# Kernel tuning notes

Measured on AMD Instinct MI355X. Metric: run time of the kernel, lower is better.

Reference implementation:

```python
import jax, jax.numpy as jnp
import numpy as np

K, MU, SIGMA = 8, 0.0, 0.1
M, N, D_DIM, T = 512, 1024, 512, 4096


def setup_inputs() -> dict:
    key = jax.random.key(0)
    ks, ke, ka, kd, kl1, kl2 = jax.random.split(key, 6)
    S = jax.random.normal(ks, (N, T), dtype=jnp.float32)
    E = jax.random.normal(ke, (M, T), dtype=jnp.float32)  # raw noise; scaled by sigma/mu in reference
    A = jax.random.uniform(ka, (M, N), dtype=jnp.float32)  # torch.rand init
    Dm = jax.random.normal(kd, (N, D_DIM), dtype=jnp.float32) / jnp.sqrt(N)  # stands in for DCT-transformed randn
    c = jnp.ones((1,), dtype=jnp.float32)
    l1 = 0.1 * jnp.abs(jax.random.normal(kl1, (1,), dtype=jnp.float32)) + 0.05
    l2 = jax.random.normal(kl2, (1,), dtype=jnp.float32)
    # LISTA params per layer; all K layers get the same closed-form init in the original
    U1 = jnp.eye(D_DIM, dtype=jnp.float32) - (1.0 / c[0]) * (Dm.T @ A.T @ A @ Dm)  # [d,d]
    V1 = (1.0 / c[0]) * (Dm.T @ A.T)  # [d,m]
    U = jnp.broadcast_to(U1, (K, D_DIM, D_DIM)).copy()
    V = jnp.broadcast_to(V1, (K, D_DIM, M)).copy()
    H0 = jnp.zeros((D_DIM, T), dtype=jnp.float32)
    return {"S": S, "E": E, "A": A, "D": Dm, "U": U, "V": V, "l1": l1, "l2": l2, "c": c, "H0": H0}


def reference(S, E, A, D, U, V, l1, l2, c, H0):
    # X = A @ S + noise (E ~ randn, scaled as in torch forward)
    X = A @ S + (E * SIGMA + MU)  # [m,T]
    # Self-attention on H0 (the original loop always feeds self.H, the zero buffer,
    # into every layer -- H is never chained). Attention map = softmax((D@H0)^T (D@H0)).
    G = D @ H0                                   # [n,T]
    attn = jax.nn.softmax(G.T @ G, axis=-1)      # [T,T]
    Z = l2[0] * (H0 @ attn)                      # [d,T]
    # All K LISTA updates share the same (H0-derived) Z and X -> batch over layers.
    mat = jnp.einsum('kde,et->kdt', U, Z) + jnp.einsum('kdm,mt->kdt', V, X)  # [K,d,T]
    thres = l1[0] / c[0]
    H_all = jnp.sign(mat) * jnp.maximum(jnp.zeros((), mat.dtype), jnp.abs(mat) - thres)
    H_last = H_all[-1]                           # only the last layer's H survives the loop
    return D @ H_last                            # S_star [n,T]
```

## Files before the change

### kernel.cpp

```cpp
#include <hip/hip_runtime.h>

typedef unsigned short ushort_t;
typedef unsigned int u32;
typedef ushort_t u16x8 __attribute__((ext_vector_type(8)));
typedef ushort_t u16x4 __attribute__((ext_vector_type(4)));
typedef __bf16   bf16x8 __attribute__((ext_vector_type(8)));
typedef float    f32x4  __attribute__((ext_vector_type(4)));

#define T_DIM 4096

__device__ __forceinline__ ushort_t f2bf(float f){
  union { float f; unsigned u; } x; x.f = f;
  unsigned r = x.u + 0x7FFFu + ((x.u >> 16) & 1u);
  return (ushort_t)(r >> 16);
}

__device__ __forceinline__ void gload16(const void* g, void* l){
  __builtin_amdgcn_global_load_lds(
      (const __attribute__((address_space(1))) u32*)g,
      (__attribute__((address_space(3))) u32*)l, 16, 0, 0);
}

__global__ __launch_bounds__(256) void prep_kernel(
    const float* __restrict__ S, const float* __restrict__ A,
    const float* __restrict__ V7, const float* __restrict__ Dm,
    ushort_t* __restrict__ St, ushort_t* __restrict__ Abf,
    ushort_t* __restrict__ Vbf, ushort_t* __restrict__ Dbf)
{
  __shared__ float tile[64][65];
  const int bid = blockIdx.x, tid = threadIdx.x;
  if (bid < 1024){
    const int t0 = (bid & 63) * 64, n0 = (bid >> 6) * 64;
#pragma unroll
    for (int i = 0; i < 4; ++i){
      int g = tid + 256 * i; int row = g >> 4, cq = g & 15;
      const f32x4 v = *(const f32x4*)&S[(size_t)(n0 + row) * T_DIM + t0 + cq * 4];
#pragma unroll
      for (int j = 0; j < 4; ++j) tile[row][cq * 4 + j] = v[j];
    }
    __syncthreads();
#pragma unroll
    for (int i = 0; i < 2; ++i){
      int g = tid + 256 * i; int tl = g >> 3, nq = g & 7;
      u16x8 h;
#pragma unroll
      for (int j = 0; j < 8; ++j) h[j] = f2bf(tile[nq * 8 + j][tl]);
      *(u16x8*)&St[(size_t)(t0 + tl) * 1024 + n0 + ((nq ^ (tl & 7)) << 3)] = h;
    }
  } else {
    int pid = bid - 1024;
    const float* src; ushort_t* dst; int g, ks;
    if (pid < 256)      { src = A;  dst = Abf; g = pid * 256 + tid;        ks = 7; }
    else if (pid < 384) { src = V7; dst = Vbf; g = (pid - 256) * 256 + tid; ks = 6; }
    else                { src = Dm; dst = Dbf; g = (pid - 384) * 256 + tid; ks = 6; }
    const int r = g >> ks, cg = g & ((1 << ks) - 1);
    const int Kd = 8 << ks;
    const size_t base = (size_t)r * Kd + (size_t)cg * 8;
    const f32x4 v0 = *(const f32x4*)&src[base];
    const f32x4 v1 = *(const f32x4*)&src[base + 4];
    u16x8 h;
#pragma unroll
    for (int j = 0; j < 4; ++j){ h[j] = f2bf(v0[j]); h[j + 4] = f2bf(v1[j]); }
    *(u16x8*)&dst[(size_t)r * Kd + ((cg >> 3) << 6) + ((((cg & 7) ^ (r & 7))) << 3)] = h;
  }
}

template<int EPI, int NK>
__global__ __launch_bounds__(512, 2) void gemm_kernel(
    const ushort_t* __restrict__ Ag, const ushort_t* __restrict__ Bg,
    void* __restrict__ Cout, const float* __restrict__ Eptr,
    const float* __restrict__ l1p, const float* __restrict__ cp)
{
  constexpr int KD = NK * 64;
  constexpr bool SWAP = (EPI != 2);
  constexpr int P = SWAP ? 2 : 4;
  constexpr int Q = SWAP ? 4 : 2;
  __shared__ __align__(16) ushort_t As[4][128 * 64];
  __shared__ __align__(16) ushort_t Bs[4][64 * 64];
  const int tid = threadIdx.x;
  const int lane = tid & 63, wid = tid >> 6;
  const int g = wid >> 2;
  const int s = wid & 3;
  const int wm = s >> 1, wn = s & 1;
  const int lr = lane & 15, lq = lane >> 4;
  const int t0 = blockIdx.x * 128, n0 = blockIdx.y * 64;
  const int ltid = tid & 255;

  f32x4 acc[P][Q];
#pragma unroll
  for (int p = 0; p < P; ++p)
#pragma unroll
    for (int q = 0; q < Q; ++q) acc[p][q] = (f32x4){0.f, 0.f, 0.f, 0.f};

  auto stage = [&](int kt){
    const int slot = ((kt & 1) << 1) | ((kt >> 1) & 1);
#pragma unroll
    for (int i = 0; i < 4; ++i){
      int c = i * 256 + ltid;
      gload16(&Ag[(size_t)(t0 + (c >> 3)) * KD + kt * 64 + (c & 7) * 8],
              &As[slot][(i * 256 + (ltid & 192)) * 8]);
    }
#pragma unroll
    for (int i = 0; i < 2; ++i){
      int c = i * 256 + ltid;
      gload16(&Bg[(size_t)(n0 + (c >> 3)) * KD + kt * 64 + (c & 7) * 8],
              &Bs[slot][(i * 256 + (ltid & 192)) * 8]);
    }
  };

  auto compute = [&](int kt){
    const int slot = ((kt & 1) << 1) | ((kt >> 1) & 1);
#pragma unroll
    for (int ksv = 0; ksv < 2; ++ksv){
      const int kb = ksv * 4 + lq;
      bf16x8 a[4], bb[2];
#pragma unroll
      for (int mf = 0; mf < 4; ++mf){
        int r = wm * 64 + mf * 16 + lr;
        a[mf] = *(const bf16x8*)&As[slot][r * 64 + ((kb ^ (r & 7)) << 3)];
      }
#pragma unroll
      for (int nf = 0; nf < 2; ++nf){
        int r = wn * 32 + nf * 16 + lr;
        bb[nf] = *(const bf16x8*)&Bs[slot][r * 64 + ((kb ^ (r & 7)) << 3)];
      }
      __builtin_amdgcn_s_setprio(1);
      if constexpr (SWAP){
#pragma unroll
        for (int nf = 0; nf < 2; ++nf)
#pragma unroll
          for (int mf = 0; mf < 4; ++mf)
            acc[nf][mf] = __builtin_amdgcn_mfma_f32_16x16x32_bf16(
                bb[nf], a[mf], acc[nf][mf], 0, 0, 0);
      } else {
#pragma unroll
        for (int mf = 0; mf < 4; ++mf)
#pragma unroll
          for (int nf = 0; nf < 2; ++nf)
            acc[mf][nf] = __builtin_amdgcn_mfma_f32_16x16x32_bf16(
                a[mf], bb[nf], acc[mf][nf], 0, 0, 0);
      }
      __builtin_amdgcn_s_setprio(0);
    }
  };

  if (g == 0){ stage(0); stage(2); }
  else       { stage(1); }

  for (int kt = 0; kt < NK; ++kt){
    if ((kt & 1) == g){
      if (kt + 2 < NK) { asm volatile("s_waitcnt vmcnt(6)" ::: "memory"); }
      else             { asm volatile("s_waitcnt vmcnt(0)" ::: "memory"); }
    }
    __builtin_amdgcn_s_barrier();
    __builtin_amdgcn_sched_barrier(0);
    if ((kt & 1) == g){
      compute(kt);
    } else {
      if (kt + 3 < NK) stage(kt + 3);
    }
  }

  float* red = (float*)&As[0][0];
  if (g == 1){
#pragma unroll
    for (int p = 0; p < P; ++p)
#pragma unroll
      for (int q = 0; q < Q; ++q)
        *(f32x4*)&red[s * 2048 + (p * Q + q) * 256 + lane * 4] = acc[p][q];
  }
  asm volatile("s_waitcnt lgkmcnt(0)" ::: "memory");
  __builtin_amdgcn_s_barrier();
  if (g == 0){
#pragma unroll
    for (int p = 0; p < P; ++p)
#pragma unroll
      for (int q = 0; q < Q; ++q){
        const f32x4 o = *(const f32x4*)&red[s * 2048 + (p * Q + q) * 256 + lane * 4];
        acc[p][q] += o;
      }

    if constexpr (EPI == 2){
      float* O = (float*)Cout;
#pragma unroll
      for (int mf = 0; mf < 4; ++mf)
#pragma unroll
        for (int nf = 0; nf < 2; ++nf){
          const int t = t0 + wm * 64 + mf * 16 + lq * 4;
          const int n = n0 + wn * 32 + nf * 16 + lr;
          *(f32x4*)&O[(size_t)n * T_DIM + t] = acc[mf][nf];
        }
    } else {
      const float thres = (EPI == 1) ? (l1p[0] / cp[0]) : 0.f;
      ushort_t* OT = (ushort_t*)Cout;
#pragma unroll
      for (int nf = 0; nf < 2; ++nf){
#pragma unroll
        for (int mf = 0; mf < 4; ++mf){
          const int m = n0 + wn * 32 + nf * 16 + lq * 4;
          const int t = t0 + wm * 64 + mf * 16 + lr;
          f32x4 v = acc[nf][mf];
          u16x4 h;
          if constexpr (EPI == 0){
#pragma unroll
            for (int j = 0; j < 4; ++j){
              float e = Eptr[(size_t)(m + j) * T_DIM + t];
              h[j] = f2bf(v[j] + 0.1f * e);
            }
          } else {
#pragma unroll
            for (int j = 0; j < 4; ++j){
              float av = fabsf(v[j]) - thres;
              float r = av > 0.f ? (v[j] > 0.f ? av : -av) : 0.f;
              h[j] = f2bf(r);
            }
          }
          *(u16x4*)&OT[(size_t)t * 512 + (m & ~63) +
                       (((((m >> 3) & 7) ^ (t & 7))) << 3) + (m & 7)] = h;
        }
      }
    }
  }
}

extern "C" void kernel_launch(void* const* d_in, const int* in_sizes, int n_in,
                              void* d_out, int out_size, void* d_ws, size_t ws_size,
                              hipStream_t stream)
{
  const float* S  = (const float*)d_in[0];
  const float* E  = (const float*)d_in[1];
  const float* A  = (const float*)d_in[2];
  const float* Dm = (const float*)d_in[3];
  const float* V  = (const float*)d_in[5];
  const float* l1 = (const float*)d_in[6];
  const float* c  = (const float*)d_in[8];

  char* ws = (char*)d_ws;
  ushort_t* St  = (ushort_t*)(ws);
  ushort_t* XT  = (ushort_t*)(ws + (size_t)( 8u << 20));
  ushort_t* HT  = (ushort_t*)(ws + (size_t)(12u << 20));
  ushort_t* Abf = (ushort_t*)(ws + (size_t)(16u << 20));
  ushort_t* Vbf = (ushort_t*)(ws + (size_t)(17u << 20));
  ushort_t* Dbf = (ushort_t*)(ws + (size_t)(17u << 20) + (512u << 10));
  const float* V7 = V + (size_t)7 * 512 * 512;

  prep_kernel<<<1664, 256, 0, stream>>>(S, A, V7, Dm, St, Abf, Vbf, Dbf);
  gemm_kernel<0, 16><<<dim3(32, 8), 512, 0, stream>>>(St, Abf, (void*)XT, E, nullptr, nullptr);
  gemm_kernel<1, 8><<<dim3(32, 8), 512, 0, stream>>>(XT, Vbf, (void*)HT, nullptr, l1, c);
  gemm_kernel<2, 8><<<dim3(32, 16), 512, 0, stream>>>(HT, Dbf, d_out, nullptr, nullptr, nullptr);
}
```

Measured before the change: 39.38 us.

## Fuse S transpose and bf16 conversion into first GEMM's staging loop

The separate prep pass that transposed S into a bf16 buffer is removed. The first GEMM now loads fp32 S tiles into registers, converts them to bf16 and writes them transposed into LDS, so the 16 MB St round trip disappears. The E noise tile is also prefetched into LDS asynchronously for the epilogue instead of being read from global memory with strided access. In exchange, staging now takes register-path loads and conversion work inside the pipelined loop, and each block adds 32 KB of LDS, which may reduce occupancy.

New measurement: 47.78 us. +21.3%, slower.

```diff
diff --git a/kernel.cpp b/kernel.cpp
--- a/kernel.cpp
+++ b/kernel.cpp
@@ -22,54 +22,175 @@
 }
 
 __global__ __launch_bounds__(256) void prep_kernel(
-    const float* __restrict__ S, const float* __restrict__ A,
-    const float* __restrict__ V7, const float* __restrict__ Dm,
-    ushort_t* __restrict__ St, ushort_t* __restrict__ Abf,
+    const float* __restrict__ A, const float* __restrict__ V7,
+    const float* __restrict__ Dm, ushort_t* __restrict__ Abf,
     ushort_t* __restrict__ Vbf, ushort_t* __restrict__ Dbf)
 {
-  __shared__ float tile[64][65];
-  const int bid = blockIdx.x, tid = threadIdx.x;
-  if (bid < 1024){
-    const int t0 = (bid & 63) * 64, n0 = (bid >> 6) * 64;
-#pragma unroll
-    for (int i = 0; i < 4; ++i){
-      int g = tid + 256 * i; int row = g >> 4, cq = g & 15;
-      const f32x4 v = *(const f32x4*)&S[(size_t)(n0 + row) * T_DIM + t0 + cq * 4];
-#pragma unroll
-      for (int j = 0; j < 4; ++j) tile[row][cq * 4 + j] = v[j];
-    }
-    __syncthreads();
+  const int pid = blockIdx.x, tid = threadIdx.x;
+  const float* src; ushort_t* dst; int g, ks;
+  if (pid < 256)      { src = A;  dst = Abf; g = pid * 256 + tid;        ks = 7; }
+  else if (pid < 384) { src = V7; dst = Vbf; g = (pid - 256) * 256 + tid; ks = 6; }
+  else                { src = Dm; dst = Dbf; g = (pid - 384) * 256 + tid; ks = 6; }
+  const int r = g >> ks, cg = g & ((1 << ks) - 1);
+  const int Kd = 8 << ks;
+  const size_t base = (size_t)r * Kd + (size_t)cg * 8;
+  const f32x4 v0 = *(const f32x4*)&src[base];
+  const f32x4 v1 = *(const f32x4*)&src[base + 4];
+  u16x8 h;
+#pragma unroll
+  for (int j = 0; j < 4; ++j){ h[j] = f2bf(v0[j]); h[j + 4] = f2bf(v1[j]); }
+  *(u16x8*)&dst[(size_t)r * Kd + ((cg >> 3) << 6) + ((((cg & 7) ^ (r & 7))) << 3)] = h;
+}
+
+__global__ __launch_bounds__(512, 2) void gemm1_kernel(
+    const float* __restrict__ S, const ushort_t* __restrict__ Bg,
+    const float* __restrict__ E, ushort_t* __restrict__ XT)
+{
+  constexpr int NK = 16;
+  __shared__ __align__(16) ushort_t As[4][128 * 64];
+  __shared__ __align__(16) ushort_t Bs[4][64 * 64];
+  __shared__ __align__(16) float Elds[64 * 128];
+  const int tid = threadIdx.x;
+  const int lane = tid & 63, wid = tid >> 6;
+  const int g = wid >> 2;
+  const int s = wid & 3;
+  const int wm = s >> 1, wn = s & 1;
+  const int lr = lane & 15, lq = lane >> 4;
+  const int t0 = blockIdx.x * 128, n0 = blockIdx.y * 64;
+  const int ltid = tid & 255;
+
+  f32x4 acc[2][4];
+#pragma unroll
+  for (int p = 0; p < 2; ++p)
+#pragma unroll
+    for (int q = 0; q < 4; ++q) acc[p][q] = (f32x4){0.f, 0.f, 0.f, 0.f};
+
+  auto stage = [&](int kt){
+    const int slot = ((kt & 1) << 1) | ((kt >> 1) & 1);
+    f32x4 rS[2][4];
 #pragma unroll
     for (int i = 0; i < 2; ++i){
-      int g = tid + 256 * i; int tl = g >> 3, nq = g & 7;
-      u16x8 h;
-#pragma unroll
-      for (int j = 0; j < 8; ++j) h[j] = f2bf(tile[nq * 8 + j][tl]);
-      *(u16x8*)&St[(size_t)(t0 + tl) * 1024 + n0 + ((nq ^ (tl & 7)) << 3)] = h;
-    }
-  } else {
-    int pid = bid - 1024;
-    const float* src; ushort_t* dst; int g, ks;
-    if (pid < 256)      { src = A;  dst = Abf; g = pid * 256 + tid;        ks = 7; }
-    else if (pid < 384) { src = V7; dst = Vbf; g = (pid - 256) * 256 + tid; ks = 6; }
-    else                { src = Dm; dst = Dbf; g = (pid - 384) * 256 + tid; ks = 6; }
-    const int r = g >> ks, cg = g & ((1 << ks) - 1);
-    const int Kd = 8 << ks;
-    const size_t base = (size_t)r * Kd + (size_t)cg * 8;
-    const f32x4 v0 = *(const f32x4*)&src[base];
-    const f32x4 v1 = *(const f32x4*)&src[base + 4];
-    u16x8 h;
-#pragma unroll
-    for (int j = 0; j < 4; ++j){ h[j] = f2bf(v0[j]); h[j + 4] = f2bf(v1[j]); }
-    *(u16x8*)&dst[(size_t)r * Kd + ((cg >> 3) << 6) + ((((cg & 7) ^ (r & 7))) << 3)] = h;
+      const int task = i * 256 + ltid, rg = task >> 5, tq = task & 31;
+#pragma unroll
+      for (int ii = 0; ii < 4; ++ii)
+        rS[i][ii] = *(const f32x4*)&S[(size_t)(kt * 64 + rg * 4 + ii) * T_DIM
+                                      + t0 + tq * 4];
+    }
+    __builtin_amdgcn_sched_barrier(0);
+#pragma unroll
+    for (int i = 0; i < 2; ++i){
+      int c = i * 256 + ltid;
+      gload16(&Bg[(size_t)(n0 + (c >> 3)) * 1024 + kt * 64 + (c & 7) * 8],
+              &Bs[slot][(i * 256 + (ltid & 192)) * 8]);
+    }
+    __builtin_amdgcn_sched_barrier(0);
+    asm volatile("s_waitcnt vmcnt(2)" ::: "memory");
+#pragma unroll
+    for (int i = 0; i < 2; ++i){
+      const int task = i * 256 + ltid, rg = task >> 5, tq = task & 31;
+#pragma unroll
+      for (int j = 0; j < 4; ++j){
+        const int t = tq * 4 + j;
+        u16x4 w;
+#pragma unroll
+        for (int ii = 0; ii < 4; ++ii) w[ii] = f2bf(rS[i][ii][j]);
+        *(u16x4*)&As[slot][t * 64 + (((rg >> 1) ^ ((t >> 1) & 7)) << 3)
+                           + ((rg & 1) << 2)] = w;
+      }
+    }
+    asm volatile("s_waitcnt lgkmcnt(0)" ::: "memory");
+  };
+
+  auto compute = [&](int kt){
+    const int slot = ((kt & 1) << 1) | ((kt >> 1) & 1);
+#pragma unroll
+    for (int ksv = 0; ksv < 2; ++ksv){
+      const int kb = ksv * 4 + lq;
+      bf16x8 a[4], bb[2];
+#pragma unroll
+      for (int mf = 0; mf < 4; ++mf){
+        int r = wm * 64 + mf * 16 + lr;
+        a[mf] = *(const bf16x8*)&As[slot][r * 64 + ((kb ^ ((r >> 1) & 7)) << 3)];
+      }
+#pragma unroll
+      for (int nf = 0; nf < 2; ++nf){
+        int r = wn * 32 + nf * 16 + lr;
+        bb[nf] = *(const bf16x8*)&Bs[slot][r * 64 + ((kb ^ (r & 7)) << 3)];
+      }
+      __builtin_amdgcn_s_setprio(1);
+#pragma unroll
+      for (int nf = 0; nf < 2; ++nf)
+#pragma unroll
+        for (int mf = 0; mf < 4; ++mf)
+          acc[nf][mf] = __builtin_amdgcn_mfma_f32_16x16x32_bf16(
+              bb[nf], a[mf], acc[nf][mf], 0, 0, 0);
+      __builtin_amdgcn_s_setprio(0);
+    }
+  };
+
+#pragma unroll
+  for (int i = 0; i < 4; ++i){
+    int c = i * 512 + tid;
+    gload16(&E[(size_t)(n0 + (c >> 5)) * T_DIM + t0 + (c & 31) * 4],
+            (char*)Elds + (size_t)(i * 512 + (tid & 448)) * 16);
+  }
+  __builtin_amdgcn_sched_barrier(0);
+  if (g == 0){ stage(0); stage(2); }
+  else       { stage(1); }
+
+  for (int kt = 0; kt < NK; ++kt){
+    __builtin_amdgcn_s_barrier();
+    __builtin_amdgcn_sched_barrier(0);
+    if ((kt & 1) == g){
+      compute(kt);
+    } else {
+      if (kt + 3 < NK) stage(kt + 3);
+      else             asm volatile("s_waitcnt vmcnt(0)" ::: "memory");
+    }
+  }
+
+  float* red = (float*)&As[0][0];
+  if (g == 1){
+#pragma unroll
+    for (int p = 0; p < 2; ++p)
+#pragma unroll
+      for (int q = 0; q < 4; ++q)
+        *(f32x4*)&red[s * 2048 + (p * 4 + q) * 256 + lane * 4] = acc[p][q];
+  }
+  asm volatile("s_waitcnt lgkmcnt(0)" ::: "memory");
+  __builtin_amdgcn_s_barrier();
+  if (g == 0){
+#pragma unroll
+    for (int p = 0; p < 2; ++p)
+#pragma unroll
+      for (int q = 0; q < 4; ++q)
+        acc[p][q] += *(const f32x4*)&red[s * 2048 + (p * 4 + q) * 256 + lane * 4];
+
+#pragma unroll
+    for (int nf = 0; nf < 2; ++nf){
+#pragma unroll
+      for (int mf = 0; mf < 4; ++mf){
+        const int m = n0 + wn * 32 + nf * 16 + lq * 4;
+        const int t = t0 + wm * 64 + mf * 16 + lr;
+        const int em = wn * 32 + nf * 16 + lq * 4;
+        const int tl = wm * 64 + mf * 16 + lr;
+        f32x4 v = acc[nf][mf];
+        u16x4 h;
+#pragma unroll
+        for (int j = 0; j < 4; ++j)
+          h[j] = f2bf(v[j] + 0.1f * Elds[(em + j) * 128 + tl]);
+        *(u16x4*)&XT[(size_t)t * 512 + (m & ~63) +
+                     (((((m >> 3) & 7) ^ (t & 7))) << 3) + (m & 7)] = h;
+      }
+    }
   }
 }
 
 template<int EPI, int NK>
 __global__ __launch_bounds__(512, 2) void gemm_kernel(
     const ushort_t* __restrict__ Ag, const ushort_t* __restrict__ Bg,
-    void* __restrict__ Cout, const float* __restrict__ Eptr,
-    const float* __restrict__ l1p, const float* __restrict__ cp)
+    void* __restrict__ Cout, const float* __restrict__ l1p,
+    const float* __restrict__ cp)
 {
   constexpr int KD = NK * 64;
   constexpr bool SWAP = (EPI != 2);
@@ -175,10 +296,8 @@
 #pragma unroll
     for (int p = 0; p < P; ++p)
 #pragma unroll
-      for (int q = 0; q < Q; ++q){
-        const f32x4 o = *(const f32x4*)&red[s * 2048 + (p * Q + q) * 256 + lane * 4];
-        acc[p][q] += o;
-      }
+      for (int q = 0; q < Q; ++q)
+        acc[p][q] += *(const f32x4*)&red[s * 2048 + (p * Q + q) * 256 + lane * 4];
 
     if constexpr (EPI == 2){
       float* O = (float*)Cout;
@@ -191,7 +310,7 @@
           *(f32x4*)&O[(size_t)n * T_DIM + t] = acc[mf][nf];
         }
     } else {
-      const float thres = (EPI == 1) ? (l1p[0] / cp[0]) : 0.f;
+      const float thres = l1p[0] / cp[0];
       ushort_t* OT = (ushort_t*)Cout;
 #pragma unroll
       for (int nf = 0; nf < 2; ++nf){
@@ -201,19 +320,11 @@
           const int t = t0 + wm * 64 + mf * 16 + lr;
           f32x4 v = acc[nf][mf];
           u16x4 h;
-          if constexpr (EPI == 0){
-#pragma unroll
-            for (int j = 0; j < 4; ++j){
-              float e = Eptr[(size_t)(m + j) * T_DIM + t];
-              h[j] = f2bf(v[j] + 0.1f * e);
-            }
-          } else {
-#pragma unroll
-            for (int j = 0; j < 4; ++j){
-              float av = fabsf(v[j]) - thres;
-              float r = av > 0.f ? (v[j] > 0.f ? av : -av) : 0.f;
-              h[j] = f2bf(r);
-            }
+#pragma unroll
+          for (int j = 0; j < 4; ++j){
+            float av = fabsf(v[j]) - thres;
+            float r = av > 0.f ? (v[j] > 0.f ? av : -av) : 0.f;
+            h[j] = f2bf(r);
           }
           *(u16x4*)&OT[(size_t)t * 512 + (m & ~63) +
                        (((((m >> 3) & 7) ^ (t & 7))) << 3) + (m & 7)] = h;
@@ -236,16 +347,15 @@
   const float* c  = (const float*)d_in[8];
 
   char* ws = (char*)d_ws;
-  ushort_t* St  = (ushort_t*)(ws);
-  ushort_t* XT  = (ushort_t*)(ws + (size_t)( 8u << 20));
-  ushort_t* HT  = (ushort_t*)(ws + (size_t)(12u << 20));
-  ushort_t* Abf = (ushort_t*)(ws + (size_t)(16u << 20));
-  ushort_t* Vbf = (ushort_t*)(ws + (size_t)(17u << 20));
-  ushort_t* Dbf = (ushort_t*)(ws + (size_t)(17u << 20) + (512u << 10));
+  ushort_t* XT  = (ushort_t*)(ws);
+  ushort_t* HT  = (ushort_t*)(ws + (size_t)( 4u << 20));
+  ushort_t* Abf = (ushort_t*)(ws + (size_t)( 8u << 20));
+  ushort_t* Vbf = (ushort_t*)(ws + (size_t)( 9u << 20));
+  ushort_t* Dbf = (ushort_t*)(ws + (size_t)(10u << 20));
   const float* V7 = V + (size_t)7 * 512 * 512;
 
-  prep_kernel<<<1664, 256, 0, stream>>>(S, A, V7, Dm, St, Abf, Vbf, Dbf);
-  gemm_kernel<0, 16><<<dim3(32, 8), 512, 0, stream>>>(St, Abf, (void*)XT, E, nullptr, nullptr);
-  gemm_kernel<1, 8><<<dim3(32, 8), 512, 0, stream>>>(XT, Vbf, (void*)HT, nullptr, l1, c);
-  gemm_kernel<2, 8><<<dim3(32, 16), 512, 0, stream>>>(HT, Dbf, d_out, nullptr, nullptr, nullptr);
-}
+  prep_kernel<<<640, 256, 0, stream>>>(A, V7, Dm, Abf, Vbf, Dbf);
+  gemm1_kernel<<<dim3(32, 8), 512, 0, stream>>>(S, Abf, E, XT);
+  gemm_kernel<1, 8><<<dim3(32, 8), 512, 0, stream>>>(XT, Vbf, (void*)HT, l1, c);
+  gemm_kernel<2, 8><<<dim3(32, 16), 512, 0, stream>>>(HT, Dbf, d_out, nullptr, nullptr);
+}
```

## Stage GEMM epilogue through LDS for coalesced stores and prefetch noise tile

Applied to the files above, without the earlier changes.

The GEMM epilogue now writes the reduced accumulators into LDS with the target swizzle applied, then has all 512 threads emit wide, contiguous global stores. Before, each lane wrote scattered 4-element fragments. For the X-producing GEMM, the noise tile E is loaded asynchronously into a new LDS buffer at kernel start, so the epilogue no longer does strided scalar global loads of E. The cost is extra LDS traffic, two more barriers in the epilogue, and an additional 32KB LDS buffer that raises shared-memory usage.

Measured after the change: 39.66 us. Within noise of the previous version (+0.7%).

```diff
diff --git a/kernel.cpp b/kernel.cpp
--- a/kernel.cpp
+++ b/kernel.cpp
@@ -77,6 +77,7 @@
   constexpr int Q = SWAP ? 4 : 2;
   __shared__ __align__(16) ushort_t As[4][128 * 64];
   __shared__ __align__(16) ushort_t Bs[4][64 * 64];
+  __shared__ __align__(16) float Elds[64 * 128];
   const int tid = threadIdx.x;
   const int lane = tid & 63, wid = tid >> 6;
   const int g = wid >> 2;
@@ -144,6 +145,15 @@
     }
   };
 
+  if constexpr (EPI == 0){
+#pragma unroll
+    for (int i = 0; i < 4; ++i){
+      int c = i * 512 + tid;
+      gload16(&Eptr[(size_t)(n0 + (c >> 5)) * T_DIM + t0 + (c & 31) * 4],
+              (char*)Elds + (size_t)(i * 512 + (tid & 448)) * 16);
+    }
+    __builtin_amdgcn_sched_barrier(0);
+  }
   if (g == 0){ stage(0); stage(2); }
   else       { stage(1); }
 
@@ -161,64 +171,95 @@
     }
   }
 
-  float* red = (float*)&As[0][0];
-  if (g == 1){
-#pragma unroll
-    for (int p = 0; p < P; ++p)
-#pragma unroll
-      for (int q = 0; q < Q; ++q)
-        *(f32x4*)&red[s * 2048 + (p * Q + q) * 256 + lane * 4] = acc[p][q];
-  }
-  asm volatile("s_waitcnt lgkmcnt(0)" ::: "memory");
-  __builtin_amdgcn_s_barrier();
-  if (g == 0){
-#pragma unroll
-    for (int p = 0; p < P; ++p)
-#pragma unroll
-      for (int q = 0; q < Q; ++q){
-        const f32x4 o = *(const f32x4*)&red[s * 2048 + (p * Q + q) * 256 + lane * 4];
-        acc[p][q] += o;
-      }
-
-    if constexpr (EPI == 2){
-      float* O = (float*)Cout;
-#pragma unroll
-      for (int mf = 0; mf < 4; ++mf)
-#pragma unroll
-        for (int nf = 0; nf < 2; ++nf){
-          const int t = t0 + wm * 64 + mf * 16 + lq * 4;
-          const int n = n0 + wn * 32 + nf * 16 + lr;
-          *(f32x4*)&O[(size_t)n * T_DIM + t] = acc[mf][nf];
-        }
-    } else {
+  float* accs = (float*)&As[0][0];
+
+  if constexpr (SWAP){
+    if (g == 1){
+#pragma unroll
+      for (int nf = 0; nf < 2; ++nf)
+#pragma unroll
+        for (int mf = 0; mf < 4; ++mf){
+          const int tl = wm * 64 + mf * 16 + lr;
+          const int em0 = wn * 32 + nf * 16 + lq * 4;
+          const int mp = (((em0 >> 3) ^ (tl & 7)) << 3) + (em0 & 7);
+          *(f32x4*)&accs[tl * 68 + mp] = acc[nf][mf];
+        }
+    }
+    asm volatile("s_waitcnt lgkmcnt(0)" ::: "memory");
+    __builtin_amdgcn_s_barrier();
+    if (g == 0){
       const float thres = (EPI == 1) ? (l1p[0] / cp[0]) : 0.f;
-      ushort_t* OT = (ushort_t*)Cout;
-#pragma unroll
-      for (int nf = 0; nf < 2; ++nf){
+#pragma unroll
+      for (int nf = 0; nf < 2; ++nf)
 #pragma unroll
         for (int mf = 0; mf < 4; ++mf){
-          const int m = n0 + wn * 32 + nf * 16 + lq * 4;
-          const int t = t0 + wm * 64 + mf * 16 + lr;
-          f32x4 v = acc[nf][mf];
-          u16x4 h;
+          const int tl = wm * 64 + mf * 16 + lr;
+          const int em0 = wn * 32 + nf * 16 + lq * 4;
+          const int mp = (((em0 >> 3) ^ (tl & 7)) << 3) + (em0 & 7);
+          f32x4 v = *(const f32x4*)&accs[tl * 68 + mp];
+          v += acc[nf][mf];
           if constexpr (EPI == 0){
 #pragma unroll
-            for (int j = 0; j < 4; ++j){
-              float e = Eptr[(size_t)(m + j) * T_DIM + t];
-              h[j] = f2bf(v[j] + 0.1f * e);
-            }
+            for (int j = 0; j < 4; ++j)
+              v[j] += 0.1f * Elds[(em0 + j) * 128 + tl];
           } else {
 #pragma unroll
             for (int j = 0; j < 4; ++j){
               float av = fabsf(v[j]) - thres;
-              float r = av > 0.f ? (v[j] > 0.f ? av : -av) : 0.f;
-              h[j] = f2bf(r);
+              v[j] = av > 0.f ? (v[j] > 0.f ? av : -av) : 0.f;
             }
           }
-          *(u16x4*)&OT[(size_t)t * 512 + (m & ~63) +
-                       (((((m >> 3) & 7) ^ (t & 7))) << 3) + (m & 7)] = h;
-        }
-      }
+          *(f32x4*)&accs[tl * 68 + mp] = v;
+        }
+    }
+    asm volatile("s_waitcnt lgkmcnt(0)" ::: "memory");
+    __builtin_amdgcn_s_barrier();
+    ushort_t* OT = (ushort_t*)Cout;
+#pragma unroll
+    for (int i = 0; i < 2; ++i){
+      const int c = i * 512 + tid;
+      const int t = c >> 3, mb = (c & 7) * 8;
+      const f32x4 a0 = *(const f32x4*)&accs[t * 68 + mb];
+      const f32x4 a1 = *(const f32x4*)&accs[t * 68 + mb + 4];
+      u16x8 h;
+#pragma unroll
+      for (int j = 0; j < 4; ++j){ h[j] = f2bf(a0[j]); h[j + 4] = f2bf(a1[j]); }
+      *(u16x8*)&OT[(size_t)(t0 + t) * 512 + n0 + mb] = h;
+    }
+  } else {
+    if (g == 1){
+#pragma unroll
+      for (int mf = 0; mf < 4; ++mf)
+#pragma unroll
+        for (int nf = 0; nf < 2; ++nf){
+          const int tl0 = wm * 64 + mf * 16 + lq * 4;
+          const int nl  = wn * 32 + nf * 16 + lr;
+          *(f32x4*)&accs[nl * 132 + tl0] = acc[mf][nf];
+        }
+    }
+    asm volatile("s_waitcnt lgkmcnt(0)" ::: "memory");
+    __builtin_amdgcn_s_barrier();
+    if (g == 0){
+#pragma unroll
+      for (int mf = 0; mf < 4; ++mf)
+#pragma unroll
+        for (int nf = 0; nf < 2; ++nf){
+          const int tl0 = wm * 64 + mf * 16 + lq * 4;
+          const int nl  = wn * 32 + nf * 16 + lr;
+          f32x4 v = *(const f32x4*)&accs[nl * 132 + tl0];
+          v += acc[mf][nf];
+          *(f32x4*)&accs[nl * 132 + tl0] = v;
+        }
+    }
+    asm volatile("s_waitcnt lgkmcnt(0)" ::: "memory");
+    __builtin_amdgcn_s_barrier();
+    float* O = (float*)Cout;
+#pragma unroll
+    for (int i = 0; i < 4; ++i){
+      const int c = i * 512 + tid;
+      const int n = c >> 5, t4 = (c & 31) * 4;
+      *(f32x4*)&O[(size_t)(n0 + n) * T_DIM + t0 + t4] =
+          *(const f32x4*)&accs[n * 132 + t4];
     }
   }
 }
```

## Fuse fp32-to-bf16 weight conversion into GEMM B-operand loads and stage E in LDS

Applied to the files above, without the earlier changes.

Removes the separate conversion of A, V7 and D to bf16 in the prep kernel. Each GEMM now loads the fp32 B operand into registers, converts it and writes swizzled bf16 into LDS inside the pipelined k-loop, using double-buffered register sets. The first GEMM also prefetches its noise tile E into LDS asynchronously before the loop, so the epilogue no longer issues strided global reads. The cost is more vmcnt bookkeeping, extra registers, and conversion work inside the main loop that is repeated by every block sharing the same weights.

Measured after the change: 53.90 us. +36.9%, slower.

```diff
diff --git a/kernel.cpp b/kernel.cpp
--- a/kernel.cpp
+++ b/kernel.cpp
@@ -22,52 +22,73 @@
 }
 
 __global__ __launch_bounds__(256) void prep_kernel(
-    const float* __restrict__ S, const float* __restrict__ A,
-    const float* __restrict__ V7, const float* __restrict__ Dm,
-    ushort_t* __restrict__ St, ushort_t* __restrict__ Abf,
-    ushort_t* __restrict__ Vbf, ushort_t* __restrict__ Dbf)
+    const float* __restrict__ S, ushort_t* __restrict__ St)
 {
   __shared__ float tile[64][65];
   const int bid = blockIdx.x, tid = threadIdx.x;
-  if (bid < 1024){
-    const int t0 = (bid & 63) * 64, n0 = (bid >> 6) * 64;
-#pragma unroll
-    for (int i = 0; i < 4; ++i){
-      int g = tid + 256 * i; int row = g >> 4, cq = g & 15;
-      const f32x4 v = *(const f32x4*)&S[(size_t)(n0 + row) * T_DIM + t0 + cq * 4];
-#pragma unroll
-      for (int j = 0; j < 4; ++j) tile[row][cq * 4 + j] = v[j];
-    }
-    __syncthreads();
-#pragma unroll
-    for (int i = 0; i < 2; ++i){
-      int g = tid + 256 * i; int tl = g >> 3, nq = g & 7;
-      u16x8 h;
-#pragma unroll
-      for (int j = 0; j < 8; ++j) h[j] = f2bf(tile[nq * 8 + j][tl]);
-      *(u16x8*)&St[(size_t)(t0 + tl) * 1024 + n0 + ((nq ^ (tl & 7)) << 3)] = h;
-    }
-  } else {
-    int pid = bid - 1024;
-    const float* src; ushort_t* dst; int g, ks;
-    if (pid < 256)      { src = A;  dst = Abf; g = pid * 256 + tid;        ks = 7; }
-    else if (pid < 384) { src = V7; dst = Vbf; g = (pid - 256) * 256 + tid; ks = 6; }
-    else                { src = Dm; dst = Dbf; g = (pid - 384) * 256 + tid; ks = 6; }
-    const int r = g >> ks, cg = g & ((1 << ks) - 1);
-    const int Kd = 8 << ks;
-    const size_t base = (size_t)r * Kd + (size_t)cg * 8;
-    const f32x4 v0 = *(const f32x4*)&src[base];
-    const f32x4 v1 = *(const f32x4*)&src[base + 4];
+  const int t0 = (bid & 63) * 64, n0 = (bid >> 6) * 64;
+#pragma unroll
+  for (int i = 0; i < 4; ++i){
+    int g = tid + 256 * i; int row = g >> 4, cq = g & 15;
+    const f32x4 v = *(const f32x4*)&S[(size_t)(n0 + row) * T_DIM + t0 + cq * 4];
+#pragma unroll
+    for (int j = 0; j < 4; ++j) tile[row][cq * 4 + j] = v[j];
+  }
+  __syncthreads();
+#pragma unroll
+  for (int i = 0; i < 2; ++i){
+    int g = tid + 256 * i; int tl = g >> 3, nq = g & 7;
     u16x8 h;
 #pragma unroll
-    for (int j = 0; j < 4; ++j){ h[j] = f2bf(v0[j]); h[j + 4] = f2bf(v1[j]); }
-    *(u16x8*)&dst[(size_t)r * Kd + ((cg >> 3) << 6) + ((((cg & 7) ^ (r & 7))) << 3)] = h;
-  }
-}
+    for (int j = 0; j < 8; ++j) h[j] = f2bf(tile[nq * 8 + j][tl]);
+    *(u16x8*)&St[(size_t)(t0 + tl) * 1024 + n0 + ((nq ^ (tl & 7)) << 3)] = h;
+  }
+}
+
+#define ISSUE_BREG(kt, rB) do {                                                \
+  _Pragma("unroll") for (int q_ = 0; q_ < 4; ++q_)                             \
+    rB[q_] = *(const f32x4*)&Bg[(size_t)(n0 + (ltid >> 2)) * KD                \
+                                + (kt) * 64 + (ltid & 3) * 16 + q_ * 4];       \
+  } while (0)
+
+#define CVT_WRITE_B(kt, rB) do {                                               \
+  const int slot_ = (((kt) & 1) << 1) | (((kt) >> 1) & 1);                     \
+  const int n_ = ltid >> 2, kq_ = ltid & 3;                                    \
+  u16x8 h0_, h1_;                                                              \
+  _Pragma("unroll") for (int j_ = 0; j_ < 4; ++j_){                            \
+    h0_[j_] = f2bf(rB[0][j_]);  h0_[j_ + 4] = f2bf(rB[1][j_]);                 \
+    h1_[j_] = f2bf(rB[2][j_]);  h1_[j_ + 4] = f2bf(rB[3][j_]);                 \
+  }                                                                            \
+  *(u16x8*)&Bs[slot_][n_ * 64 + (((kq_ * 2) ^ (n_ & 7)) << 3)] = h0_;          \
+  *(u16x8*)&Bs[slot_][n_ * 64 + (((kq_ * 2 + 1) ^ (n_ & 7)) << 3)] = h1_;      \
+  } while (0)
+
+#define STEP(kt, RWR, RISS) do {                                               \
+  if (((kt) & 1) == g){                                                        \
+    if ((kt) + 2 < NK) { asm volatile("s_waitcnt vmcnt(8)" ::: "memory"); }    \
+    else               { asm volatile("s_waitcnt vmcnt(0)" ::: "memory"); }    \
+    __builtin_amdgcn_s_barrier();                                              \
+    __builtin_amdgcn_sched_barrier(0);                                         \
+    compute(kt);                                                               \
+  } else {                                                                     \
+    if ((kt) + 3 < NK) ISSUE_BREG((kt) + 3, RISS);                             \
+    __builtin_amdgcn_s_barrier();                                              \
+    if ((kt) + 3 < NK){                                                        \
+      issueA((kt) + 3);                                                        \
+      asm volatile("s_waitcnt vmcnt(12)" ::: "memory");                        \
+    } else if ((kt) + 1 < NK){                                                 \
+      asm volatile("s_waitcnt vmcnt(4)" ::: "memory");                         \
+    } else {                                                                   \
+      asm volatile("s_waitcnt vmcnt(0)" ::: "memory");                         \
+    }                                                                          \
+    __builtin_amdgcn_sched_barrier(0);                                         \
+    if ((kt) + 1 < NK) CVT_WRITE_B((kt) + 1, RWR);                             \
+    asm volatile("s_waitcnt lgkmcnt(0)" ::: "memory");                         \
+  } } while (0)
 
 template<int EPI, int NK>
 __global__ __launch_bounds__(512, 2) void gemm_kernel(
-    const ushort_t* __restrict__ Ag, const ushort_t* __restrict__ Bg,
+    const ushort_t* __restrict__ Ag, const float* __restrict__ Bg,
     void* __restrict__ Cout, const float* __restrict__ Eptr,
     const float* __restrict__ l1p, const float* __restrict__ cp)
 {
@@ -77,6 +98,7 @@
   constexpr int Q = SWAP ? 4 : 2;
   __shared__ __align__(16) ushort_t As[4][128 * 64];
   __shared__ __align__(16) ushort_t Bs[4][64 * 64];
+  __shared__ __align__(16) float Elds[(EPI == 0) ? 8192 : 4];
   const int tid = threadIdx.x;
   const int lane = tid & 63, wid = tid >> 6;
   const int g = wid >> 2;
@@ -92,7 +114,9 @@
 #pragma unroll
     for (int q = 0; q < Q; ++q) acc[p][q] = (f32x4){0.f, 0.f, 0.f, 0.f};
 
-  auto stage = [&](int kt){
+  f32x4 rBa[4], rBb[4];
+
+  auto issueA = [&](int kt){
     const int slot = ((kt & 1) << 1) | ((kt >> 1) & 1);
 #pragma unroll
     for (int i = 0; i < 4; ++i){
@@ -100,12 +124,6 @@
       gload16(&Ag[(size_t)(t0 + (c >> 3)) * KD + kt * 64 + (c & 7) * 8],
               &As[slot][(i * 256 + (ltid & 192)) * 8]);
     }
-#pragma unroll
-    for (int i = 0; i < 2; ++i){
-      int c = i * 256 + ltid;
-      gload16(&Bg[(size_t)(n0 + (c >> 3)) * KD + kt * 64 + (c & 7) * 8],
-              &Bs[slot][(i * 256 + (ltid & 192)) * 8]);
-    }
   };
 
   auto compute = [&](int kt){
@@ -144,21 +162,31 @@
     }
   };
 
-  if (g == 0){ stage(0); stage(2); }
-  else       { stage(1); }
-
-  for (int kt = 0; kt < NK; ++kt){
-    if ((kt & 1) == g){
-      if (kt + 2 < NK) { asm volatile("s_waitcnt vmcnt(6)" ::: "memory"); }
-      else             { asm volatile("s_waitcnt vmcnt(0)" ::: "memory"); }
-    }
-    __builtin_amdgcn_s_barrier();
+  if constexpr (EPI == 0){
+#pragma unroll
+    for (int i = 0; i < 4; ++i){
+      int c = i * 512 + tid;
+      gload16(&Eptr[(size_t)(n0 + (c >> 5)) * T_DIM + t0 + (c & 31) * 4],
+              (char*)Elds + (size_t)(i * 512 + (tid & 448)) * 16);
+    }
     __builtin_amdgcn_sched_barrier(0);
-    if ((kt & 1) == g){
-      compute(kt);
-    } else {
-      if (kt + 3 < NK) stage(kt + 3);
-    }
+  }
+  if (g == 0){
+    ISSUE_BREG(0, rBa); issueA(0);
+    asm volatile("s_waitcnt vmcnt(4)" ::: "memory");
+    CVT_WRITE_B(0, rBa);
+    ISSUE_BREG(2, rBa); issueA(2);
+  } else {
+    ISSUE_BREG(1, rBa); issueA(1);
+  }
+  asm volatile("s_waitcnt lgkmcnt(0)" ::: "memory");
+
+#pragma unroll 1
+  for (int kt0 = 0; kt0 < NK; kt0 += 4){
+    STEP(kt0 + 0, rBa, rBb);
+    STEP(kt0 + 1, rBa, rBb);
+    STEP(kt0 + 2, rBb, rBa);
+    STEP(kt0 + 3, rBb, rBa);
   }
 
   float* red = (float*)&As[0][0];
@@ -175,10 +203,8 @@
 #pragma unroll
     for (int p = 0; p < P; ++p)
 #pragma unroll
-      for (int q = 0; q < Q; ++q){
-        const f32x4 o = *(const f32x4*)&red[s * 2048 + (p * Q + q) * 256 + lane * 4];
-        acc[p][q] += o;
-      }
+      for (int q = 0; q < Q; ++q)
+        acc[p][q] += *(const f32x4*)&red[s * 2048 + (p * Q + q) * 256 + lane * 4];
 
     if constexpr (EPI == 2){
       float* O = (float*)Cout;
@@ -199,14 +225,14 @@
         for (int mf = 0; mf < 4; ++mf){
           const int m = n0 + wn * 32 + nf * 16 + lq * 4;
           const int t = t0 + wm * 64 + mf * 16 + lr;
+          const int em0 = wn * 32 + nf * 16 + lq * 4;
+          const int tl  = wm * 64 + mf * 16 + lr;
           f32x4 v = acc[nf][mf];
           u16x4 h;
           if constexpr (EPI == 0){
 #pragma unroll
-            for (int j = 0; j < 4; ++j){
-              float e = Eptr[(size_t)(m + j) * T_DIM + t];
-              h[j] = f2bf(v[j] + 0.1f * e);
-            }
+            for (int j = 0; j < 4; ++j)
+              h[j] = f2bf(v[j] + 0.1f * Elds[(em0 + j) * 128 + tl]);
           } else {
 #pragma unroll
             for (int j = 0; j < 4; ++j){
@@ -236,16 +262,13 @@
   const float* c  = (const float*)d_in[8];
 
   char* ws = (char*)d_ws;
-  ushort_t* St  = (ushort_t*)(ws);
-  ushort_t* XT  = (ushort_t*)(ws + (size_t)( 8u << 20));
-  ushort_t* HT  = (ushort_t*)(ws + (size_t)(12u << 20));
-  ushort_t* Abf = (ushort_t*)(ws + (size_t)(16u << 20));
-  ushort_t* Vbf = (ushort_t*)(ws + (size_t)(17u << 20));
-  ushort_t* Dbf = (ushort_t*)(ws + (size_t)(17u << 20) + (512u << 10));
+  ushort_t* St = (ushort_t*)(ws);
+  ushort_t* XT = (ushort_t*)(ws + (size_t)( 8u << 20));
+  ushort_t* HT = (ushort_t*)(ws + (size_t)(12u << 20));
   const float* V7 = V + (size_t)7 * 512 * 512;
 
-  prep_kernel<<<1664, 256, 0, stream>>>(S, A, V7, Dm, St, Abf, Vbf, Dbf);
-  gemm_kernel<0, 16><<<dim3(32, 8), 512, 0, stream>>>(St, Abf, (void*)XT, E, nullptr, nullptr);
-  gemm_kernel<1, 8><<<dim3(32, 8), 512, 0, stream>>>(XT, Vbf, (void*)HT, nullptr, l1, c);
-  gemm_kernel<2, 8><<<dim3(32, 16), 512, 0, stream>>>(HT, Dbf, d_out, nullptr, nullptr, nullptr);
-}
+  prep_kernel<<<1024, 256, 0, stream>>>(S, St);
+  gemm_kernel<0, 16><<<dim3(32, 8), 512, 0, stream>>>(St, A, (void*)XT, E, nullptr, nullptr);
+  gemm_kernel<1, 8><<<dim3(32, 8), 512, 0, stream>>>(XT, V7, (void*)HT, nullptr, l1, c);
+  gemm_kernel<2, 8><<<dim3(32, 16), 512, 0, stream>>>(HT, Dm, d_out, nullptr, nullptr, nullptr);
+}
```
